# Kernel optimization log

Hardware: AMD Instinct MI355X
Metric: run time of the kernel (lower is better)

The kernel has to match this reference:

```python
import jax, jax.numpy as jnp
import numpy as np

BETA = 0.9
ITER = 2


def setup_inputs() -> dict:
    key = jax.random.key(0)
    B, items, E = 8, 32, 128
    N = B * items * items  # 8192 pairs
    k1, k2 = jax.random.split(key)
    pairs = jax.random.normal(k1, (N, E), dtype=jnp.float32)
    # scale W so bilinear scores don't saturate sigmoid (init faithfulness not required)
    W = jax.random.normal(k2, (E, E), dtype=jnp.float32) / jnp.sqrt(jnp.float32(E))
    cond = jnp.ones((B, items, items), dtype=jnp.int32)  # all pairs valid (dense nonzero)
    # map_pair[b,i,j] = row-major linear index into `pairs`, matching torch.nonzero order
    map_pair = jnp.arange(N, dtype=jnp.int32).reshape(B, items, items)
    return {"pairs": pairs, "W": W, "cond": cond, "map_pair": map_pair}


def reference(pairs, W, cond, map_pair):
    B, items = map_pair.shape[0], map_pair.shape[1]
    N, E = pairs.shape
    # torch.nonzero of the broadcast [B,items,items,items] cond; cond is dense (all nonzero),
    # so nonzeros enumerate all (b,i,j,k) in row-major order.
    bi, ii, ji, ki = [x.reshape(-1) for x in jnp.indices((B, items, items, items))]
    part1 = map_pair[bi, ii, ki]  # pair (i,k)
    part2 = map_pair[bi, ki, ji]  # pair (k,j)
    valid = (part1 >= 0) & (part2 >= 0)  # [N*items]
    # static -inf masks (loop-invariant)
    eq_mask = ((ji == ki) | (ii == ki)).reshape(N, items)  # idx2==idx3 or idx1==idx3
    ar = jnp.arange(items)
    diag_idx = map_pair[:, ar, ar].reshape(-1)  # self-pairs (i,i) -> rows of N
    row_mask = jnp.zeros((N,), dtype=bool).at[diag_idx].set(True)
    inf_mask = eq_mask | row_mask[:, None]  # [N, items]
    neg_inf = jnp.float32(-jnp.inf)

    for _ in range(ITER):
        # generate: bilinear then gather
        bilin = pairs @ W  # [N, E]
        a = jnp.where(valid[:, None], bilin[part1], 0.0).reshape(N, items, E)
        b = jnp.where(valid[:, None], pairs[part2], 0.0).reshape(N, items, E)
        new_pairs = a * b  # [N, items, E]
        # aggregate: masked -inf fills
        new_pairs = jnp.where(inf_mask[:, :, None], neg_inf, new_pairs)
        zero_mask = jnp.all(new_pairs == 0.0, axis=2)  # [N, items]
        new_pairs = jnp.where(zero_mask[:, :, None], neg_inf, new_pairs)
        # interpolation gate: 1 where all walks are masked, beta otherwise
        mat = jnp.where(jnp.all(jnp.isinf(new_pairs), axis=1), 1.0, jnp.float32(BETA))  # [N, E]
        new = jnp.sum(jax.nn.sigmoid(new_pairs), axis=1)  # sigmoid(-inf)=0; [N, E]
        pairs = mat * pairs + (1.0 - mat) * new
    return pairs
```

## Files before the change

### kernel.cpp

```cpp
#include <hip/hip_runtime.h>

typedef __attribute__((ext_vector_type(8))) short bf16x8;
typedef __attribute__((ext_vector_type(4))) float f32x4;

#define NEG_LOG2E (-1.4426950408889634f)

__device__ __forceinline__ short f2bf(float f) {
    unsigned u = __float_as_uint(f);
    unsigned r = (u + 0x7FFFu + ((u >> 16) & 1u)) >> 16;
    return (short)r;
}

__global__ __launch_bounds__(256) void prep(
    const float* __restrict__ pairs,
    const float* __restrict__ W,
    short* __restrict__ pbf,
    short* __restrict__ WTs)
{
    const int t = threadIdx.x, blk = blockIdx.x;
    if (blk < 64) {
        int idx = blk * 256 + t;
        int k = idx >> 7, n = idx & 127;
        WTs[n * 128 + k] = f2bf(NEG_LOG2E * W[idx]);
    } else {
        int f = (blk - 64) * 256 + t;
        float4 v = ((const float4*)pairs)[f];
        union { short s[4]; unsigned long long u; } pk;
        pk.s[0] = f2bf(v.x); pk.s[1] = f2bf(v.y);
        pk.s[2] = f2bf(v.z); pk.s[3] = f2bf(v.w);
        *(unsigned long long*)(pbf + (size_t)f * 4) = pk.u;
    }
}

__global__ __launch_bounds__(512, 6) void walk_iter(
    const float* __restrict__ srcF,
    const short* __restrict__ srcB,
    const short* __restrict__ WTs,
    float* __restrict__ dstF,
    short* __restrict__ dstB)
{
    __shared__ float G[32][132];

    const int t  = threadIdx.x;
    const int bi = blockIdx.x >> 1;
    const int jg = blockIdx.x & 1;
    const int b  = bi >> 5;
    const int i  = bi & 31;

    const int j  = jg * 16 + (t >> 5);
    const int g  = t & 31, e0 = g << 2;

    const float* pb = srcF + ((size_t)(b * 32) * 32 + j) * 128 + e0;
    float4 pA = *(const float4*)pb;

    {
        const int wv = t >> 6, l = t & 63;
        const int m0 = (wv & 1) * 16;
        const int lm = l & 15, quad = l >> 4;
        const int n0 = (wv >> 1) * 16;
        const short* arow = srcB + (size_t)(bi * 32 + m0 + lm) * 128;
        const short* brow = WTs + (size_t)(n0 + lm) * 128;
        f32x4 acc0 = {0.f, 0.f, 0.f, 0.f};
        f32x4 acc1 = {0.f, 0.f, 0.f, 0.f};
        #pragma unroll
        for (int kb = 0; kb < 4; ++kb) {
            int ko = kb * 32 + quad * 8;
            bf16x8 af  = *(const bf16x8*)(arow + ko);
            bf16x8 bf0 = *(const bf16x8*)(brow + ko);
            bf16x8 bf1 = *(const bf16x8*)(brow + 64 * 128 + ko);
            acc0 = __builtin_amdgcn_mfma_f32_16x16x32_bf16(af, bf0, acc0, 0, 0, 0);
            acc1 = __builtin_amdgcn_mfma_f32_16x16x32_bf16(af, bf1, acc1, 0, 0, 0);
        }
        #pragma unroll
        for (int r = 0; r < 4; ++r) {
            G[m0 + quad * 4 + r][n0 + lm]      = acc0[r];
            G[m0 + quad * 4 + r][n0 + 64 + lm] = acc1[r];
        }
    }
    __syncthreads();

    float4 sacc = make_float4(0.f, 0.f, 0.f, 0.f);
    if (i != j) {
        const float* pn = pb + 4096;
        float4 pB = *(const float4*)pn;
        #pragma unroll 4
        for (int k = 0; k < 32; ++k) {
            float4 p = pA;
            pA = pB;
            if (k < 30) { pn += 4096; pB = *(const float4*)pn; }
            float4 gg = *(const float4*)&G[k][e0];
            float t0 = gg.x * p.x, t1 = gg.y * p.y;
            float t2 = gg.z * p.z, t3 = gg.w * p.w;
            float x0 = __builtin_amdgcn_exp2f(t0);
            float x1 = __builtin_amdgcn_exp2f(t1);
            float x2 = __builtin_amdgcn_exp2f(t2);
            float x3 = __builtin_amdgcn_exp2f(t3);
            float d0 = 1.0f + x0, d1 = 1.0f + x1;
            float d2 = 1.0f + x2, d3 = 1.0f + x3;
            float d01 = d0 * d1, d23 = d2 * d3;
            float r = __builtin_amdgcn_rcpf(d01 * d23);
            r = ((k == i) | (k == j)) ? 0.0f : r;
            float r01 = r * d23, r23 = r * d01;
            sacc.x = fmaf(r01, d1, sacc.x);
            sacc.y = fmaf(r01, d0, sacc.y);
            sacc.z = fmaf(r23, d3, sacc.z);
            sacc.w = fmaf(r23, d2, sacc.w);
        }
    }

    const float matv = (i == j) ? 1.0f : 0.9f;
    const float om   = 1.0f - matv;
    const size_t orow = ((size_t)bi * 32 + j) * 128 + e0;
    float4 pr = *(const float4*)(srcF + orow);
    float4 o;
    o.x = fmaf(om, sacc.x, matv * pr.x);
    o.y = fmaf(om, sacc.y, matv * pr.y);
    o.z = fmaf(om, sacc.z, matv * pr.z);
    o.w = fmaf(om, sacc.w, matv * pr.w);
    *(float4*)(dstF + orow) = o;

    if (dstB) {
        union { short s[4]; unsigned long long u; } pk;
        pk.s[0] = f2bf(o.x); pk.s[1] = f2bf(o.y);
        pk.s[2] = f2bf(o.z); pk.s[3] = f2bf(o.w);
        *(unsigned long long*)(dstB + orow) = pk.u;
    }
}

extern "C" void kernel_launch(void* const* d_in, const int* in_sizes, int n_in,
                              void* d_out, int out_size, void* d_ws, size_t ws_size,
                              hipStream_t stream) {
    (void)in_sizes; (void)n_in; (void)out_size; (void)ws_size;
    const float* pairs = (const float*)d_in[0];
    const float* W     = (const float*)d_in[1];
    char* ws = (char*)d_ws;
    short* WTs   = (short*)ws;
    short* pbf   = (short*)(ws + (1 << 16));
    float* tmp   = (float*)(ws + (1 << 16) + (1 << 21));
    short* tmpbf = (short*)(ws + (1 << 16) + (1 << 21) + (1 << 22));
    float* out = (float*)d_out;

    prep<<<1088, 256, 0, stream>>>(pairs, W, pbf, WTs);
    walk_iter<<<512, 512, 0, stream>>>(pairs, pbf, WTs, tmp, tmpbf);
    walk_iter<<<512, 512, 0, stream>>>(tmp,   tmpbf, WTs, out, nullptr);
}
```

Before: 94.92 us.

## Deepen global prefetch ring, prefetch LDS rows, and remap block order

Replaces the two-deep prefetch of pair rows with a four-entry register ring, and loads the next LDS row of G one iteration ahead. The k-loop is fully unrolled. Block indexing is changed so consecutive blocks walk across batches rather than across i within a batch, which alters L2 locality for the shared pair(k,j) rows. Launch bounds are relaxed from 6 to 4 waves per SIMD to leave room for the extra registers, at the cost of lower occupancy.

```diff
diff --git a/kernel.cpp b/kernel.cpp
--- a/kernel.cpp
+++ b/kernel.cpp
@@ -32,7 +32,7 @@
     }
 }
 
-__global__ __launch_bounds__(512, 6) void walk_iter(
+__global__ __launch_bounds__(512, 4) void walk_iter(
     const float* __restrict__ srcF,
     const short* __restrict__ srcB,
     const short* __restrict__ WTs,
@@ -42,16 +42,21 @@
     __shared__ float G[32][132];
 
     const int t  = threadIdx.x;
-    const int bi = blockIdx.x >> 1;
-    const int jg = blockIdx.x & 1;
-    const int b  = bi >> 5;
-    const int i  = bi & 31;
+    const int blk = blockIdx.x;
+    const int b  = blk & 7;
+    const int i  = (blk >> 3) & 31;
+    const int jg = blk >> 8;
+    const int bi = b * 32 + i;
 
     const int j  = jg * 16 + (t >> 5);
     const int g  = t & 31, e0 = g << 2;
 
-    const float* pb = srcF + ((size_t)(b * 32) * 32 + j) * 128 + e0;
-    float4 pA = *(const float4*)pb;
+    const float* pb = srcF + ((size_t)(b * 1024) + j) * 128 + e0;
+    float4 ring[4];
+    ring[0] = *(const float4*)(pb);
+    ring[1] = *(const float4*)(pb + 4096);
+    ring[2] = *(const float4*)(pb + 2 * 4096);
+    ring[3] = *(const float4*)(pb + 3 * 4096);
 
     {
         const int wv = t >> 6, l = t & 63;
@@ -81,14 +86,14 @@
 
     float4 sacc = make_float4(0.f, 0.f, 0.f, 0.f);
     if (i != j) {
-        const float* pn = pb + 4096;
-        float4 pB = *(const float4*)pn;
-        #pragma unroll 4
+        float4 gg = *(const float4*)&G[0][e0];
+        #pragma unroll
         for (int k = 0; k < 32; ++k) {
-            float4 p = pA;
-            pA = pB;
-            if (k < 30) { pn += 4096; pB = *(const float4*)pn; }
-            float4 gg = *(const float4*)&G[k][e0];
+            float4 p = ring[k & 3];
+            if (k + 4 < 32)
+                ring[k & 3] = *(const float4*)(pb + (size_t)(k + 4) * 4096);
+            float4 gn;
+            if (k + 1 < 32) gn = *(const float4*)&G[k + 1][e0];
             float t0 = gg.x * p.x, t1 = gg.y * p.y;
             float t2 = gg.z * p.z, t3 = gg.w * p.w;
             float x0 = __builtin_amdgcn_exp2f(t0);
@@ -105,6 +110,7 @@
             sacc.y = fmaf(r01, d0, sacc.y);
             sacc.z = fmaf(r23, d3, sacc.z);
             sacc.w = fmaf(r23, d2, sacc.w);
+            gg = gn;
         }
     }
 
```

Result: slower. 98.64 us (+3.9%).
